# Kernel tuning notes

Hardware: AMD Instinct MI355X
Metric: run time of the kernel (lower is better)

The kernel has to match this reference:

```python
import jax, jax.numpy as jnp
import numpy as np

B, T, H, W, E, V, K = 16, 64, 16, 32, 256, 128, 3
NUM_BLOCKS = 3


def setup_inputs() -> dict:
    key = jax.random.key(0)
    ks = jax.random.split(key, 8)
    sc = 0.05  # keep logits moderate
    return {
        "encoder_output": jax.random.normal(ks[0], (B, H, W, E), jnp.float32),
        "decoder_input": jax.random.normal(ks[1], (B, H, W, E), jnp.float32),
        "labels": jax.random.randint(ks[2], (B, T), 0, V),
        "embed_table": (jax.random.normal(ks[3], (V, E), jnp.float32) * sc),
        "conv_w": (jax.random.normal(ks[4], (K, E, 2 * E), jnp.float32) * sc),  # ConvTBC weight [k, Cin, Cout]
        "conv_b": jnp.zeros((2 * E,), jnp.float32),
        "W_w": (jax.random.normal(ks[5], (E, E), jnp.float32) * sc),   # Linear(out/2 -> E), torch layout [out,in]
        "W_b": jnp.zeros((E,), jnp.float32),
        "Wo_w": (jax.random.normal(ks[6], (V, E), jnp.float32) * sc),  # Linear(E -> V)
        "Wo_b": jnp.zeros((V,), jnp.float32),
    }


def reference(encoder_output, decoder_input, embed_table, conv_w, conv_b,
              W_w, W_b, Wo_w, Wo_b, labels):
    # Work in [B, T, C]; the torch code's TBC transposes are layout-only.
    s = embed_table[labels]                     # [B, T, E]  (s in original, kept fixed)
    a = s                                       # a_l
    dec_flat = decoder_input.reshape(B, H * W, E)            # [B, HW, E]
    residual = (encoder_output + decoder_input).reshape(B, H * W, E)  # [B, HW, E]

    for _ in range(NUM_BLOCKS):
        # ConvTBC: 1D conv over T, weight [k, Cin, Cout]
        conv = jax.lax.conv_general_dilated(
            a, conv_w, window_strides=(1,), padding=((K // 2, K // 2),),
            dimension_numbers=("NWC", "WIO", "NWC")) + conv_b   # [B, T, 2E]
        # GLU over channel dim
        za, zb = jnp.split(conv, 2, axis=-1)
        z = za * jax.nn.sigmoid(zb)                              # [B, T, E]
        h = z @ W_w.T + W_b + s                                  # [B, T, E]
        # exp / sum over spatial positions == softmax over HW (same math, stable)
        scores = jnp.einsum("bte,bse->bts", h, dec_flat)         # [B, T, HW]
        alpha = jax.nn.softmax(scores, axis=2)
        # weighted sum of residual (avoids the [B,T,HW,E] repeat)
        c = jnp.einsum("bts,bse->bte", alpha, residual)          # [B, T, E]
        a = c + z

    logits = a @ Wo_w.T + Wo_b                                   # [B, T, V]
    return jax.nn.log_softmax(logits, axis=2)


if __name__ == "__main__":
    out = reference(**setup_inputs())
    print(out.shape)
```

## Files before the change

kernel.cpp:

```cpp
#include <hip/hip_runtime.h>
#include <hip/hip_bf16.h>
#include <math.h>

#define BB 16
#define TT 64
#define HWXY 512
#define EE 256
#define VV 128

typedef __bf16 bf16x8 __attribute__((ext_vector_type(8)));
typedef unsigned short u16x8 __attribute__((ext_vector_type(8)));
typedef float f32x4 __attribute__((ext_vector_type(4)));
typedef unsigned short u16;

__device__ __forceinline__ f32x4 mfma16(bf16x8 a, bf16x8 b, f32x4 c) {
    return __builtin_amdgcn_mfma_f32_16x16x32_bf16(a, b, c, 0, 0, 0);
}

__device__ __forceinline__ unsigned short f2bf(float f) {
    union { float f; unsigned int i; } v; v.f = f;
    unsigned int x = v.i;
    return (unsigned short)((x + 0x7fffu + ((x >> 16) & 1u)) >> 16);
}

__device__ __forceinline__ float bf2f(unsigned short u) {
    union { unsigned int i; float f; } v; v.i = ((unsigned int)u) << 16;
    return v.f;
}

__device__ __forceinline__ u16x8 pack8(float4 v0, float4 v1) {
    u16x8 o;
    o[0] = f2bf(v0.x); o[1] = f2bf(v0.y); o[2] = f2bf(v0.z); o[3] = f2bf(v0.w);
    o[4] = f2bf(v1.x); o[5] = f2bf(v1.y); o[6] = f2bf(v1.z); o[7] = f2bf(v1.w);
    return o;
}

__device__ __forceinline__ void dma16(const void* g, void* l) {
    __builtin_amdgcn_global_load_lds(
        (const __attribute__((address_space(1))) void*)g,
        (__attribute__((address_space(3))) void*)l, 16, 0, 0);
}

#define VMWAIT0() do { asm volatile("s_waitcnt vmcnt(0)" ::: "memory"); \
                       __builtin_amdgcn_sched_barrier(0); } while (0)

__global__ __launch_bounds__(256) void k_setup(
    const float* __restrict__ enc, const float* __restrict__ dec,
    const int* __restrict__ labels, const float* __restrict__ embed,
    const float* __restrict__ conv_w, const float* __restrict__ W_w,
    const float* __restrict__ Wo_w,
    u16* __restrict__ s_bf, u16* __restrict__ dec_bf, u16* __restrict__ resT,
    u16* __restrict__ convwT, u16* __restrict__ WT, u16* __restrict__ Wo_bf) {
    __shared__ unsigned short tl[64][66];
    int bid = blockIdx.x;
    if (bid < 512) {
        const int b = bid >> 5, rem = bid & 31;
        const int s0 = (rem >> 2) << 6, e0 = (rem & 3) << 6;
#pragma unroll
        for (int it = 0; it < 16; ++it) {
            int lin = threadIdx.x + it * 256;
            int sl = lin >> 6, el = lin & 63;
            int src = (b * HWXY + s0 + sl) * EE + e0 + el;
            float dv = dec[src];
            dec_bf[src] = f2bf(dv);
            tl[sl][el] = f2bf(enc[src] + dv);
        }
        __syncthreads();
#pragma unroll
        for (int it = 0; it < 16; ++it) {
            int lin = threadIdx.x + it * 256;
            int el = lin >> 6, sl = lin & 63;
            resT[(b * EE + e0 + el) * HWXY + s0 + sl] = tl[sl][el];
        }
        return;
    }
    bid -= 512;
    if (bid < 96) {
        const int c0 = (bid >> 3) << 6, j0 = (bid & 7) << 6;
#pragma unroll
        for (int it = 0; it < 16; ++it) {
            int lin = threadIdx.x + it * 256;
            int cl = lin >> 6, jl = lin & 63;
            tl[cl][jl] = f2bf(conv_w[(c0 + cl) * 512 + j0 + jl]);
        }
        __syncthreads();
#pragma unroll
        for (int it = 0; it < 16; ++it) {
            int lin = threadIdx.x + it * 256;
            int jl = lin >> 6, cl = lin & 63;
            convwT[(j0 + jl) * 768 + c0 + cl] = tl[cl][jl];
        }
        return;
    }
    bid -= 96;
    if (bid < 16) {
        const int c0 = (bid >> 2) << 6, j0 = (bid & 3) << 6;
#pragma unroll
        for (int it = 0; it < 16; ++it) {
            int lin = threadIdx.x + it * 256;
            int cl = lin >> 6, jl = lin & 63;
            tl[cl][jl] = f2bf(W_w[(c0 + cl) * 256 + j0 + jl]);
        }
        __syncthreads();
#pragma unroll
        for (int it = 0; it < 16; ++it) {
            int lin = threadIdx.x + it * 256;
            int el = lin >> 6, pl = lin & 63;
            WT[(j0 + el) * 256 + c0 + pl] = tl[pl][el];
        }
        return;
    }
    bid -= 16;
    int i8 = (bid * 256 + threadIdx.x) * 8;
    const int n1 = BB * TT * EE;
    if (i8 < n1) {
        int b = i8 >> 14, t = (i8 >> 8) & 63, e = i8 & 255;
        int lab = labels[b * TT + t];
        const float* ep = embed + lab * EE + e;
        float4 v0 = *(const float4*)ep, v1 = *(const float4*)(ep + 4);
        *(u16x8*)(s_bf + i8) = pack8(v0, v1);
        return;
    }
    i8 -= n1;
    float4 v0 = *(const float4*)(Wo_w + i8), v1 = *(const float4*)(Wo_w + i8 + 4);
    *(u16x8*)(Wo_bf + i8) = pack8(v0, v1);
}

__global__ __launch_bounds__(256) void k_precomp(
    const u16* __restrict__ dec_bf, const u16* __restrict__ WT,
    const u16* __restrict__ s_bf, const float* __restrict__ W_b,
    u16* __restrict__ G, float* __restrict__ base_g,
    const u16* __restrict__ convwT, const float* __restrict__ conv_b,
    u16* __restrict__ z_bf) {
    __shared__ __align__(16) char smem[98304];
    char* const As = smem;
    char* const Bs = smem + 32768;
    const int tid = threadIdx.x;
    const int w = tid >> 6, L = tid & 63, l16 = L & 15, lg = L >> 4;
    int bid = blockIdx.x;

    if (bid < 256) {
        const int b = bid >> 4, st = (bid >> 1) & 7, et = bid & 1;
#pragma unroll
        for (int i = 0; i < 8; ++i) {
            const int p = w * 8 + i;
            const int r = 2 * p + (L >> 5);
            dma16(dec_bf + (b * HWXY + st * 64 + r) * EE + (((L & 31) ^ (r & 7)) << 3),
                  As + p * 1024);
        }
#pragma unroll
        for (int i = 0; i < 16; ++i) {
            const int slot = w * 16 + i;
            const int kc = slot >> 3, nf = slot & 7;
            dma16(WT + (et * 128 + nf * 16 + l16) * EE + kc * 32 + lg * 8,
                  Bs + slot * 1024);
        }
        VMWAIT0();
        __syncthreads();
        f32x4 acc[4][2] = {{{0,0,0,0},{0,0,0,0}},{{0,0,0,0},{0,0,0,0}},
                           {{0,0,0,0},{0,0,0,0}},{{0,0,0,0},{0,0,0,0}}};
#pragma unroll
        for (int kc = 0; kc < 8; ++kc) {
#pragma unroll
            for (int m = 0; m < 4; ++m) {
                const int arow = m * 16 + l16;
                const bf16x8 af = *(const bf16x8*)(
                    As + arow * 512 + (((kc * 4 + lg) ^ (arow & 7)) << 4));
                acc[m][0] = mfma16(af, *(const bf16x8*)(Bs + (kc * 8 + w * 2) * 1024 + L * 16), acc[m][0]);
                acc[m][1] = mfma16(af, *(const bf16x8*)(Bs + (kc * 8 + w * 2 + 1) * 1024 + L * 16), acc[m][1]);
            }
        }
#pragma unroll
        for (int m = 0; m < 4; ++m)
#pragma unroll
            for (int nf = 0; nf < 2; ++nf)
#pragma unroll
                for (int j = 0; j < 4; ++j) {
                    const int s = st * 64 + m * 16 + lg * 4 + j;
                    const int e = et * 128 + w * 32 + nf * 16 + l16;
                    G[(b * HWXY + s) * EE + e] = f2bf(acc[m][nf][j]);
                }
        return;
    }
    if (bid < 384) {
        bid -= 256;
        const int b = bid >> 3, st = bid & 7;
#pragma unroll
        for (int it = 0; it < 8; ++it) {
            int unit = tid + it * 256;
            int row = unit >> 5, ch = unit & 31;
            u16x8 v = *(const u16x8*)(s_bf + (b * TT + row) * EE + ch * 8);
            u16x8 o;
#pragma unroll
            for (int k = 0; k < 8; ++k) o[k] = f2bf(bf2f(v[k]) + W_b[ch * 8 + k]);
            *(u16x8*)(As + row * 512 + ((ch ^ (row & 7)) << 4)) = o;
        }
#pragma unroll
        for (int i = 0; i < 8; ++i) {
            const int slot = w * 8 + i;
            const int kc = slot >> 2, nf = slot & 3;
            dma16(dec_bf + (b * HWXY + st * 64 + nf * 16 + l16) * EE + kc * 32 + lg * 8,
                  Bs + slot * 1024);
        }
        VMWAIT0();
        __syncthreads();
        f32x4 acc[4] = {{0,0,0,0},{0,0,0,0},{0,0,0,0},{0,0,0,0}};
        const int arow = w * 16 + l16;
#pragma unroll
        for (int kc = 0; kc < 8; ++kc) {
            const bf16x8 af = *(const bf16x8*)(
                As + arow * 512 + (((kc * 4 + lg) ^ (arow & 7)) << 4));
#pragma unroll
            for (int nf = 0; nf < 4; ++nf)
                acc[nf] = mfma16(af, *(const bf16x8*)(Bs + (kc * 4 + nf) * 1024 + L * 16), acc[nf]);
        }
#pragma unroll
        for (int nf = 0; nf < 4; ++nf)
#pragma unroll
            for (int j = 0; j < 4; ++j) {
                const int t = w * 16 + lg * 4 + j;
                base_g[(b * TT + t) * HWXY + st * 64 + nf * 16 + l16] = acc[nf][j];
            }
        return;
    }
    {
        bid -= 384;
        const int ct = bid >> 4, b = bid & 15;
        char* const Ac = smem;
        char* const Bc = smem + 33792;
#pragma unroll
        for (int i = 0; i < 12; ++i) {
            const int slot = w * 12 + i;
            const int kc = slot >> 1, half = slot & 1;
            dma16(convwT + (ct * 16 + l16 + half * 256) * 768 + kc * 32 + lg * 8,
                  Bc + slot * 1024);
        }
#pragma unroll
        for (int i = 0; i < 8; ++i) {
            const int p = w * 8 + i;
            const int r = 1 + 2 * p + (L >> 5);
            dma16(s_bf + (b * TT + r - 1) * EE + (((L & 31) ^ (r & 7)) << 3),
                  Ac + 512 + p * 1024);
        }
        if (tid < 64) {
            char* dst = (tid < 32) ? (Ac + tid * 16) : (Ac + 65 * 512 + (tid - 32) * 16);
            *(u16x8*)dst = (u16x8){0,0,0,0,0,0,0,0};
        }
        VMWAIT0();
        __syncthreads();

        f32x4 za = {0,0,0,0}, zb = {0,0,0,0};
#pragma unroll
        for (int kt = 0; kt < 3; ++kt) {
            const int arow = w * 16 + l16 + kt;
            const char* ab = Ac + arow * 512;
            const int swz = (arow & 7) << 4;
#pragma unroll
            for (int ec = 0; ec < 8; ++ec) {
                const bf16x8 af = *(const bf16x8*)(ab + ((ec * 64 + lg * 16) ^ swz));
                const int kc = kt * 8 + ec;
                za = mfma16(af, *(const bf16x8*)(Bc + (kc * 2) * 1024 + L * 16), za);
                zb = mfma16(af, *(const bf16x8*)(Bc + (kc * 2 + 1) * 1024 + L * 16), zb);
            }
        }
        const int p = ct * 16 + l16;
        const float cbA = conv_b[p], cbB = conv_b[p + 256];
#pragma unroll
        for (int j = 0; j < 4; ++j) {
            const int t = w * 16 + lg * 4 + j;
            const float v = za[j] + cbA, u = zb[j] + cbB;
            z_bf[(b * TT + t) * EE + p] = f2bf(v / (1.0f + __expf(-u)));
        }
    }
}

__global__ __launch_bounds__(256) void k_conv(
    const u16* __restrict__ a_in, const u16* __restrict__ convwT,
    const float* __restrict__ conv_b, u16* __restrict__ z_bf) {
    __shared__ __align__(16) char As[33792];
    __shared__ __align__(16) char Bs[49152];
    const int b = blockIdx.x, ct = blockIdx.y;
    const int tid = threadIdx.x;
    const int w = tid >> 6, L = tid & 63, l16 = L & 15, lg = L >> 4;

#pragma unroll
    for (int i = 0; i < 12; ++i) {
        const int slot = w * 12 + i;
        const int kc = slot >> 1, half = slot & 1;
        dma16(convwT + (ct * 16 + l16 + half * 256) * 768 + kc * 32 + lg * 8,
              Bs + slot * 1024);
    }
#pragma unroll
    for (int i = 0; i < 8; ++i) {
        const int p = w * 8 + i;
        const int r = 1 + 2 * p + (L >> 5);
        dma16(a_in + (b * TT + r - 1) * EE + (((L & 31) ^ (r & 7)) << 3),
              As + 512 + p * 1024);
    }
    if (tid < 64) {
        char* dst = (tid < 32) ? (As + tid * 16) : (As + 65 * 512 + (tid - 32) * 16);
        *(u16x8*)dst = (u16x8){0,0,0,0,0,0,0,0};
    }
    VMWAIT0();
    __syncthreads();

    f32x4 za = {0,0,0,0}, zb = {0,0,0,0};
#pragma unroll
    for (int kt = 0; kt < 3; ++kt) {
        const int arow = w * 16 + l16 + kt;
        const char* ab = As + arow * 512;
        const int swz = (arow & 7) << 4;
#pragma unroll
        for (int ec = 0; ec < 8; ++ec) {
            const bf16x8 af = *(const bf16x8*)(ab + ((ec * 64 + lg * 16) ^ swz));
            const int kc = kt * 8 + ec;
            za = mfma16(af, *(const bf16x8*)(Bs + (kc * 2) * 1024 + L * 16), za);
            zb = mfma16(af, *(const bf16x8*)(Bs + (kc * 2 + 1) * 1024 + L * 16), zb);
        }
    }
    const int p = ct * 16 + l16;
    const float cbA = conv_b[p], cbB = conv_b[p + 256];
#pragma unroll
    for (int j = 0; j < 4; ++j) {
        const int t = w * 16 + lg * 4 + j;
        const float v = za[j] + cbA, u = zb[j] + cbB;
        z_bf[(b * TT + t) * EE + p] = f2bf(v / (1.0f + __expf(-u)));
    }
}

__global__ __launch_bounds__(256) void k_scores(
    const u16* __restrict__ z_bf, const u16* __restrict__ G,
    const float* __restrict__ base_g, u16* __restrict__ p_bf,
    float* __restrict__ m_part, float* __restrict__ s_part) {
    __shared__ __align__(16) char Zs[32768];
    __shared__ __align__(16) char Gs[16384];
    __shared__ float basel[64 * 36];
    const int b = blockIdx.x, st = blockIdx.y;
    const int tid = threadIdx.x;
    const int w = tid >> 6, L = tid & 63, l16 = L & 15, lg = L >> 4;

#pragma unroll
    for (int i = 0; i < 8; ++i) {
        const int p = w * 8 + i;
        const int r = 2 * p + (L >> 5);
        dma16(z_bf + (b * TT + r) * EE + (((L & 31) ^ (r & 7)) << 3), Zs + p * 1024);
    }
#pragma unroll
    for (int i = 0; i < 4; ++i) {
        const int slot = w * 4 + i;
        const int kc = slot >> 1, nf = slot & 1;
        dma16(G + (b * HWXY + st * 32 + nf * 16 + l16) * EE + kc * 32 + lg * 8,
              Gs + slot * 1024);
    }
    {
        const int row = tid >> 2, c0 = (tid & 3) * 8;
        const float* src = base_g + (b * TT + row) * HWXY + st * 32 + c0;
        float4 v0 = *(const float4*)src, v1 = *(const float4*)(src + 4);
        *(float4*)(basel + row * 36 + c0) = v0;
        *(float4*)(basel + row * 36 + c0 + 4) = v1;
    }
    VMWAIT0();
    __syncthreads();

    f32x4 sc[2] = {{0,0,0,0},{0,0,0,0}};
    const int arow = w * 16 + l16;
#pragma unroll
    for (int kc = 0; kc < 8; ++kc) {
        const bf16x8 af = *(const bf16x8*)(
            Zs + arow * 512 + (((kc * 4 + lg) ^ (arow & 7)) << 4));
        sc[0] = mfma16(af, *(const bf16x8*)(Gs + (kc * 2) * 1024 + L * 16), sc[0]);
        sc[1] = mfma16(af, *(const bf16x8*)(Gs + (kc * 2 + 1) * 1024 + L * 16), sc[1]);
    }
    float pm[4], ps[4];
#pragma unroll
    for (int j = 0; j < 4; ++j) {
        const int row = w * 16 + lg * 4 + j;
        sc[0][j] += basel[row * 36 + l16];
        sc[1][j] += basel[row * 36 + 16 + l16];
        float m = fmaxf(sc[0][j], sc[1][j]);
#pragma unroll
        for (int off = 8; off >= 1; off >>= 1) m = fmaxf(m, __shfl_xor(m, off));
        pm[j] = m;
        const float p0 = __expf(sc[0][j] - m);
        const float p1 = __expf(sc[1][j] - m);
        sc[0][j] = p0; sc[1][j] = p1;
        float s = p0 + p1;
#pragma unroll
        for (int off = 8; off >= 1; off >>= 1) s += __shfl_xor(s, off);
        ps[j] = s;
    }
    if (l16 == 0) {
#pragma unroll
        for (int j = 0; j < 4; ++j) {
            const int t = w * 16 + lg * 4 + j;
            m_part[(b * 16 + st) * TT + t] = pm[j];
            s_part[(b * 16 + st) * TT + t] = ps[j];
        }
    }
#pragma unroll
    for (int nf = 0; nf < 2; ++nf)
#pragma unroll
        for (int j = 0; j < 4; ++j) {
            const int t = w * 16 + lg * 4 + j;
            p_bf[(b * TT + t) * HWXY + st * 32 + nf * 16 + l16] = f2bf(sc[nf][j]);
        }
}

__global__ __launch_bounds__(256) void k_attn(
    const u16* __restrict__ p_bf, const u16* __restrict__ resT,
    const u16* __restrict__ z_bf, const float* __restrict__ m_part,
    const float* __restrict__ s_part, u16* __restrict__ a_out) {
    __shared__ __align__(16) char Ps[32768];
    __shared__ __align__(16) char Bs[32768];
    __shared__ u16 Zr[1024];
    __shared__ float mp[512], sp[512];
    const int b = blockIdx.x, et = blockIdx.y, tt = blockIdx.z;
    const int tid = threadIdx.x;
    const int w = tid >> 6, L = tid & 63, l16 = L & 15, lg = L >> 4;

#pragma unroll
    for (int i = 0; i < 8; ++i) {
        const int r = w * 8 + i;
        dma16(p_bf + (b * TT + tt * 32 + r) * HWXY + ((L ^ (r & 7)) << 3), Ps + r * 1024);
    }
#pragma unroll
    for (int i = 0; i < 8; ++i) {
        const int slot = w * 8 + i;
        const int kc = slot >> 1, nf = slot & 1;
        dma16(resT + (b * EE + et * 32 + nf * 16 + l16) * HWXY + kc * 32 + lg * 8,
              Bs + slot * 1024);
    }
    {
        if (tid < 128) {
            const int t = tid >> 2, part = tid & 3;
            *(u16x8*)(Zr + t * 32 + part * 8) =
                *(const u16x8*)(z_bf + (b * TT + tt * 32 + t) * EE + et * 32 + part * 8);
        }
        const int stl = tid >> 5, tl = tid & 31;
        mp[tid] = m_part[(b * 16 + stl) * TT + tt * 32 + tl];
        sp[tid] = s_part[(b * 16 + stl) * TT + tt * 32 + tl];
        mp[tid + 256] = m_part[(b * 16 + stl + 8) * TT + tt * 32 + tl];
        sp[tid + 256] = s_part[(b * 16 + stl + 8) * TT + tt * 32 + tl];
    }
    VMWAIT0();
    __syncthreads();

    const int mg = w >> 1, nh = w & 1;
    float corr[4][16];
#pragma unroll
    for (int j = 0; j < 4; ++j) {
        const int row = mg * 16 + lg * 4 + j;
        float mgl = mp[row];
#pragma unroll
        for (int s = 1; s < 16; ++s) mgl = fmaxf(mgl, mp[s * 32 + row]);
        float S = 0.f;
#pragma unroll
        for (int s = 0; s < 16; ++s) {
            const float c = __expf(mp[s * 32 + row] - mgl);
            corr[j][s] = c;
            S += sp[s * 32 + row] * c;
        }
        const float is = 1.0f / S;
#pragma unroll
        for (int s = 0; s < 16; ++s) corr[j][s] *= is;
    }

    f32x4 ca = {0,0,0,0};
    const int arow = mg * 16 + l16;
#pragma unroll
    for (int st = 0; st < 16; ++st) {
        const bf16x8 af = *(const bf16x8*)(
            Ps + arow * 1024 + (((st * 4 + lg) ^ (arow & 7)) << 4));
        f32x4 t0 = mfma16(af, *(const bf16x8*)(Bs + (st * 2 + nh) * 1024 + L * 16),
                          (f32x4){0,0,0,0});
#pragma unroll
        for (int j = 0; j < 4; ++j) ca[j] += t0[j] * corr[j][st];
    }
#pragma unroll
    for (int j = 0; j < 4; ++j) {
        const int row = mg * 16 + lg * 4 + j;
        const int t = tt * 32 + row;
        a_out[(b * TT + t) * EE + et * 32 + nh * 16 + l16] =
            f2bf(ca[j] + bf2f(Zr[row * 32 + nh * 16 + l16]));
    }
}

__global__ __launch_bounds__(256) void k_logits(
    const u16* __restrict__ a_bf, const u16* __restrict__ Wo_bf,
    const float* __restrict__ Wo_b, float* __restrict__ out) {
    __shared__ __align__(16) char As[8192];
    __shared__ __align__(16) char Ws[65536];
    __shared__ float red_m[64], red_s[64];
    const int b = blockIdx.x, tt = blockIdx.y;
    const int tid = threadIdx.x;
    const int w = tid >> 6, L = tid & 63, l16 = L & 15, lg = L >> 4;

#pragma unroll
    for (int i = 0; i < 2; ++i) {
        const int p = w * 2 + i;
        const int row = p * 2 + (L >> 5);
        dma16(a_bf + (b * TT + tt * 16 + row) * EE + (((L & 31) ^ (row & 7)) << 3),
              As + p * 1024);
    }
#pragma unroll
    for (int i = 0; i < 16; ++i) {
        const int slot = w * 16 + i;
        const int kc = slot >> 3, vg = slot & 7;
        dma16(Wo_bf + (vg * 16 + l16) * EE + kc * 32 + lg * 8, Ws + slot * 1024);
    }
    VMWAIT0();
    __syncthreads();

    f32x4 l0 = {0,0,0,0}, l1 = {0,0,0,0};
#pragma unroll
    for (int kc = 0; kc < 8; ++kc) {
        const bf16x8 af = *(const bf16x8*)(As + l16 * 512 + ((kc * 64 + lg * 16) ^ ((l16 & 7) << 4)));
        l0 = mfma16(af, *(const bf16x8*)(Ws + (kc * 8 + w * 2) * 1024 + L * 16), l0);
        l1 = mfma16(af, *(const bf16x8*)(Ws + (kc * 8 + w * 2 + 1) * 1024 + L * 16), l1);
    }
    const int v0 = w * 32 + l16, v1 = v0 + 16;
    const float wb0 = Wo_b[v0], wb1 = Wo_b[v1];
    float lv0[4], lv1[4], mg[4];
#pragma unroll
    for (int j = 0; j < 4; ++j) {
        lv0[j] = l0[j] + wb0;
        lv1[j] = l1[j] + wb1;
        float m = fmaxf(lv0[j], lv1[j]);
#pragma unroll
        for (int off = 8; off >= 1; off >>= 1) m = fmaxf(m, __shfl_xor(m, off));
        if (l16 == 0) red_m[(lg * 4 + j) * 4 + w] = m;
    }
    __syncthreads();
#pragma unroll
    for (int j = 0; j < 4; ++j) {
        const int row = lg * 4 + j;
        float m = red_m[row * 4 + 0];
#pragma unroll
        for (int ww = 1; ww < 4; ++ww) m = fmaxf(m, red_m[row * 4 + ww]);
        mg[j] = m;
        float s = __expf(lv0[j] - m) + __expf(lv1[j] - m);
#pragma unroll
        for (int off = 8; off >= 1; off >>= 1) s += __shfl_xor(s, off);
        if (l16 == 0) red_s[row * 4 + w] = s;
    }
    __syncthreads();
#pragma unroll
    for (int j = 0; j < 4; ++j) {
        const int row = lg * 4 + j;
        float s = red_s[row * 4 + 0] + red_s[row * 4 + 1] + red_s[row * 4 + 2] + red_s[row * 4 + 3];
        const float lse = mg[j] + __logf(s);
        const int gt = b * TT + tt * 16 + row;
        out[gt * VV + v0] = lv0[j] - lse;
        out[gt * VV + v1] = lv1[j] - lse;
    }
}

extern "C" void kernel_launch(void* const* d_in, const int* in_sizes, int n_in,
                              void* d_out, int out_size, void* d_ws, size_t ws_size,
                              hipStream_t stream) {
    const float* enc    = (const float*)d_in[0];
    const float* dec    = (const float*)d_in[1];
    const int*   labels = (const int*)d_in[2];
    const float* embed  = (const float*)d_in[3];
    const float* conv_w = (const float*)d_in[4];
    const float* conv_b = (const float*)d_in[5];
    const float* W_w    = (const float*)d_in[6];
    const float* W_b    = (const float*)d_in[7];
    const float* Wo_w   = (const float*)d_in[8];
    const float* Wo_b   = (const float*)d_in[9];
    float* out = (float*)d_out;
    char* ws = (char*)d_ws;

    u16*   a0     = (u16*)(ws + 0x000000);
    u16*   a1     = (u16*)(ws + 0x080000);
    u16*   s_bf   = (u16*)(ws + 0x100000);
    u16*   dec_bf = (u16*)(ws + 0x180000);
    u16*   resT   = (u16*)(ws + 0x580000);
    u16*   convwT = (u16*)(ws + 0x980000);
    u16*   WT     = (u16*)(ws + 0xA40000);
    u16*   Wo_bf  = (u16*)(ws + 0xA60000);
    u16*   z_bf   = (u16*)(ws + 0xA80000);
    u16*   p_bf   = (u16*)(ws + 0xB00000);
    float* m_part = (float*)(ws + 0xC00000);
    float* s_part = (float*)(ws + 0xC10000);
    float* base_g = (float*)(ws + 0xC20000);
    u16*   G      = (u16*)(ws + 0xE20000);

    k_setup<<<768, 256, 0, stream>>>(enc, dec, labels, embed, conv_w, W_w, Wo_w,
                                     s_bf, dec_bf, resT, convwT, WT, Wo_bf);
    k_precomp<<<640, 256, 0, stream>>>(dec_bf, WT, s_bf, W_b, G, base_g,
                                       convwT, conv_b, z_bf);

    k_scores<<<dim3(16, 16), 256, 0, stream>>>(z_bf, G, base_g, p_bf, m_part, s_part);
    k_attn<<<dim3(16, 8, 2), 256, 0, stream>>>(p_bf, resT, z_bf, m_part, s_part, a1);

    k_conv<<<dim3(16, 16), 256, 0, stream>>>(a1, convwT, conv_b, z_bf);
    k_scores<<<dim3(16, 16), 256, 0, stream>>>(z_bf, G, base_g, p_bf, m_part, s_part);
    k_attn<<<dim3(16, 8, 2), 256, 0, stream>>>(p_bf, resT, z_bf, m_part, s_part, a0);

    k_conv<<<dim3(16, 16), 256, 0, stream>>>(a0, convwT, conv_b, z_bf);
    k_scores<<<dim3(16, 16), 256, 0, stream>>>(z_bf, G, base_g, p_bf, m_part, s_part);
    k_attn<<<dim3(16, 8, 2), 256, 0, stream>>>(p_bf, resT, z_bf, m_part, s_part, a1);

    k_logits<<<dim3(16, 4), 256, 0, stream>>>(a1, Wo_bf, Wo_b, out);
}
```

Before: 66.31 us.

## Fuse scores, softmax and attention into one flash-style kernel per block

Replaces the separate scores and attention kernels with one kernel. Each workgroup handles 16 time steps of one batch over all 512 spatial positions. It computes the scores, does the full softmax in registers with cross-wave reductions through LDS, then multiplies by the residual, double-buffering G and resT tiles with async global-to-LDS loads. This removes the p_bf, m_part and s_part round trips through global memory and three kernel launches. The cost is a grid of only 64 workgroups with about 107KB of LDS each, so most of the GPU's compute units sit idle.

Result: slower. 95.41 us (+43.9%).

```diff
diff --git a/kernel.cpp b/kernel.cpp
--- a/kernel.cpp
+++ b/kernel.cpp
@@ -41,8 +41,13 @@
         (__attribute__((address_space(3))) void*)l, 16, 0, 0);
 }
 
-#define VMWAIT0() do { asm volatile("s_waitcnt vmcnt(0)" ::: "memory"); \
+#define VMWAIT(N) do { asm volatile("s_waitcnt vmcnt(" #N ")" ::: "memory"); \
                        __builtin_amdgcn_sched_barrier(0); } while (0)
+#define VMWAIT0() VMWAIT(0)
+
+__device__ __forceinline__ void frag_store(char* lds, int col, int row, unsigned short v) {
+    *(unsigned short*)(lds + ((col >> 3) << 8) + row * 16 + ((col & 7) << 1)) = v;
+}
 
 __global__ __launch_bounds__(256) void k_setup(
     const float* __restrict__ enc, const float* __restrict__ dec,
@@ -328,160 +333,144 @@
     }
 }
 
-__global__ __launch_bounds__(256) void k_scores(
+__global__ __launch_bounds__(256) void k_sattn(
     const u16* __restrict__ z_bf, const u16* __restrict__ G,
-    const float* __restrict__ base_g, u16* __restrict__ p_bf,
-    float* __restrict__ m_part, float* __restrict__ s_part) {
-    __shared__ __align__(16) char Zs[32768];
-    __shared__ __align__(16) char Gs[16384];
-    __shared__ float basel[64 * 36];
-    const int b = blockIdx.x, st = blockIdx.y;
+    const float* __restrict__ base_g, const u16* __restrict__ resT,
+    u16* __restrict__ a_out) {
+    __shared__ __align__(16) char smem[107008];
+    char* const zs = smem;
+    float* const red_m = (float*)(smem + 8192);
+    float* const red_s = (float*)(smem + 8448);
+    char* const pb = smem + 8704;
+    char* const big = smem + 41472;
+
+    const int b = blockIdx.x, t0 = blockIdx.y << 4;
     const int tid = threadIdx.x;
     const int w = tid >> 6, L = tid & 63, l16 = L & 15, lg = L >> 4;
-
-#pragma unroll
-    for (int i = 0; i < 8; ++i) {
-        const int p = w * 8 + i;
-        const int r = 2 * p + (L >> 5);
-        dma16(z_bf + (b * TT + r) * EE + (((L & 31) ^ (r & 7)) << 3), Zs + p * 1024);
-    }
-#pragma unroll
-    for (int i = 0; i < 4; ++i) {
-        const int slot = w * 4 + i;
-        const int kc = slot >> 1, nf = slot & 1;
-        dma16(G + (b * HWXY + st * 32 + nf * 16 + l16) * EE + kc * 32 + lg * 8,
-              Gs + slot * 1024);
-    }
-    {
-        const int row = tid >> 2, c0 = (tid & 3) * 8;
-        const float* src = base_g + (b * TT + row) * HWXY + st * 32 + c0;
-        float4 v0 = *(const float4*)src, v1 = *(const float4*)(src + 4);
-        *(float4*)(basel + row * 36 + c0) = v0;
-        *(float4*)(basel + row * 36 + c0 + 4) = v1;
-    }
-    VMWAIT0();
-    __syncthreads();
-
-    f32x4 sc[2] = {{0,0,0,0},{0,0,0,0}};
-    const int arow = w * 16 + l16;
-#pragma unroll
-    for (int kc = 0; kc < 8; ++kc) {
-        const bf16x8 af = *(const bf16x8*)(
-            Zs + arow * 512 + (((kc * 4 + lg) ^ (arow & 7)) << 4));
-        sc[0] = mfma16(af, *(const bf16x8*)(Gs + (kc * 2) * 1024 + L * 16), sc[0]);
-        sc[1] = mfma16(af, *(const bf16x8*)(Gs + (kc * 2 + 1) * 1024 + L * 16), sc[1]);
-    }
-    float pm[4], ps[4];
-#pragma unroll
-    for (int j = 0; j < 4; ++j) {
-        const int row = w * 16 + lg * 4 + j;
-        sc[0][j] += basel[row * 36 + l16];
-        sc[1][j] += basel[row * 36 + 16 + l16];
-        float m = fmaxf(sc[0][j], sc[1][j]);
+    char* const myg = big + w * 8192;
+
+    dma16(z_bf + (b * TT + t0 + l16) * EE + (w * 2) * 32 + lg * 8, zs + (w * 2) * 1024);
+    dma16(z_bf + (b * TT + t0 + l16) * EE + (w * 2 + 1) * 32 + lg * 8, zs + (w * 2 + 1) * 1024);
+#pragma unroll
+    for (int c = 0; c < 8; ++c)
+        dma16(base_g + (b * TT + t0 + (L >> 2)) * HWXY + c * 64 + w * 16 + (L & 3) * 4,
+              pb + c * 4096 + w * 1024);
+#pragma unroll
+    for (int c = 0; c < 2; ++c)
+#pragma unroll
+        for (int kc = 0; kc < 8; ++kc)
+            dma16(G + (b * HWXY + c * 64 + w * 16 + l16) * EE + kc * 32 + lg * 8,
+                  myg + c * 32768 + kc * 1024);
+    VMWAIT(16);
+    __syncthreads();
+
+    f32x4 sc[8] = {{0,0,0,0},{0,0,0,0},{0,0,0,0},{0,0,0,0},
+                   {0,0,0,0},{0,0,0,0},{0,0,0,0},{0,0,0,0}};
+#pragma unroll
+    for (int c = 0; c < 8; ++c) {
+        if (c < 7) { VMWAIT(8); } else { VMWAIT(0); }
+#pragma unroll
+        for (int kc = 0; kc < 8; ++kc) {
+            const bf16x8 af = *(const bf16x8*)(zs + kc * 1024 + L * 16);
+            const bf16x8 bfr = *(const bf16x8*)(myg + (c & 1) * 32768 + kc * 1024 + L * 16);
+            sc[c] = mfma16(af, bfr, sc[c]);
+        }
+        if (c < 6)
+#pragma unroll
+            for (int kc = 0; kc < 8; ++kc)
+                dma16(G + (b * HWXY + (c + 2) * 64 + w * 16 + l16) * EE + kc * 32 + lg * 8,
+                      myg + (c & 1) * 32768 + kc * 1024);
+    }
+#pragma unroll
+    for (int c = 0; c < 8; ++c)
+#pragma unroll
+        for (int j = 0; j < 4; ++j)
+            sc[c][j] += *(const float*)(pb + c * 4096 + w * 1024 +
+                                        (lg * 4 + j) * 64 + (l16 >> 2) * 16 + (l16 & 3) * 4);
+#pragma unroll
+    for (int c = 0; c < 2; ++c)
+#pragma unroll
+        for (int q = 0; q < 8; ++q) {
+            const int kc = q >> 2, nf = q & 3;
+            dma16(resT + (b * EE + w * 64 + nf * 16 + l16) * HWXY + c * 64 + kc * 32 + lg * 8,
+                  myg + c * 32768 + q * 1024);
+        }
+
+#pragma unroll
+    for (int j = 0; j < 4; ++j) {
+        float m = sc[0][j];
+#pragma unroll
+        for (int c = 1; c < 8; ++c) m = fmaxf(m, sc[c][j]);
 #pragma unroll
         for (int off = 8; off >= 1; off >>= 1) m = fmaxf(m, __shfl_xor(m, off));
-        pm[j] = m;
-        const float p0 = __expf(sc[0][j] - m);
-        const float p1 = __expf(sc[1][j] - m);
-        sc[0][j] = p0; sc[1][j] = p1;
-        float s = p0 + p1;
+        if (l16 == 0) red_m[(lg * 4 + j) * 4 + w] = m;
+    }
+    __syncthreads();
+    float inv[4];
+#pragma unroll
+    for (int j = 0; j < 4; ++j) {
+        const int row = lg * 4 + j;
+        const float m = fmaxf(fmaxf(red_m[row * 4 + 0], red_m[row * 4 + 1]),
+                              fmaxf(red_m[row * 4 + 2], red_m[row * 4 + 3]));
+        float s = 0.f;
+#pragma unroll
+        for (int c = 0; c < 8; ++c) {
+            const float p = __expf(sc[c][j] - m);
+            sc[c][j] = p;
+            s += p;
+        }
 #pragma unroll
         for (int off = 8; off >= 1; off >>= 1) s += __shfl_xor(s, off);
-        ps[j] = s;
-    }
-    if (l16 == 0) {
+        if (l16 == 0) red_s[row * 4 + w] = s;
+    }
+    __syncthreads();
+#pragma unroll
+    for (int j = 0; j < 4; ++j) {
+        const int row = lg * 4 + j;
+        inv[j] = 1.0f / (red_s[row * 4 + 0] + red_s[row * 4 + 1] +
+                         red_s[row * 4 + 2] + red_s[row * 4 + 3]);
+    }
+#pragma unroll
+    for (int c = 0; c < 8; ++c) {
+        const int col = c * 64 + w * 16 + l16;
+#pragma unroll
+        for (int j = 0; j < 4; ++j)
+            frag_store(pb, col, lg * 4 + j, f2bf(sc[c][j]));
+    }
+    __syncthreads();
+
+    f32x4 acc[4] = {{0,0,0,0},{0,0,0,0},{0,0,0,0},{0,0,0,0}};
+#pragma unroll
+    for (int c = 0; c < 8; ++c) {
+        if (c < 7) { VMWAIT(8); } else { VMWAIT(0); }
+#pragma unroll
+        for (int kc = 0; kc < 2; ++kc) {
+            const bf16x8 af = *(const bf16x8*)(pb + (c * 2 + kc) * 1024 + L * 16);
+#pragma unroll
+            for (int nf = 0; nf < 4; ++nf) {
+                const bf16x8 bfr = *(const bf16x8*)(
+                    myg + (c & 1) * 32768 + (kc * 4 + nf) * 1024 + L * 16);
+                acc[nf] = mfma16(af, bfr, acc[nf]);
+            }
+        }
+        if (c < 6)
+#pragma unroll
+            for (int q = 0; q < 8; ++q) {
+                const int kc = q >> 2, nf = q & 3;
+                dma16(resT + (b * EE + w * 64 + nf * 16 + l16) * HWXY + (c + 2) * 64 + kc * 32 + lg * 8,
+                      myg + (c & 1) * 32768 + q * 1024);
+            }
+    }
+
+#pragma unroll
+    for (int nf = 0; nf < 4; ++nf) {
+        const int e = w * 64 + nf * 16 + l16;
 #pragma unroll
         for (int j = 0; j < 4; ++j) {
-            const int t = w * 16 + lg * 4 + j;
-            m_part[(b * 16 + st) * TT + t] = pm[j];
-            s_part[(b * 16 + st) * TT + t] = ps[j];
-        }
-    }
-#pragma unroll
-    for (int nf = 0; nf < 2; ++nf)
-#pragma unroll
-        for (int j = 0; j < 4; ++j) {
-            const int t = w * 16 + lg * 4 + j;
-            p_bf[(b * TT + t) * HWXY + st * 32 + nf * 16 + l16] = f2bf(sc[nf][j]);
-        }
-}
-
-__global__ __launch_bounds__(256) void k_attn(
-    const u16* __restrict__ p_bf, const u16* __restrict__ resT,
-    const u16* __restrict__ z_bf, const float* __restrict__ m_part,
-    const float* __restrict__ s_part, u16* __restrict__ a_out) {
-    __shared__ __align__(16) char Ps[32768];
-    __shared__ __align__(16) char Bs[32768];
-    __shared__ u16 Zr[1024];
-    __shared__ float mp[512], sp[512];
-    const int b = blockIdx.x, et = blockIdx.y, tt = blockIdx.z;
-    const int tid = threadIdx.x;
-    const int w = tid >> 6, L = tid & 63, l16 = L & 15, lg = L >> 4;
-
-#pragma unroll
-    for (int i = 0; i < 8; ++i) {
-        const int r = w * 8 + i;
-        dma16(p_bf + (b * TT + tt * 32 + r) * HWXY + ((L ^ (r & 7)) << 3), Ps + r * 1024);
-    }
-#pragma unroll
-    for (int i = 0; i < 8; ++i) {
-        const int slot = w * 8 + i;
-        const int kc = slot >> 1, nf = slot & 1;
-        dma16(resT + (b * EE + et * 32 + nf * 16 + l16) * HWXY + kc * 32 + lg * 8,
-              Bs + slot * 1024);
-    }
-    {
-        if (tid < 128) {
-            const int t = tid >> 2, part = tid & 3;
-            *(u16x8*)(Zr + t * 32 + part * 8) =
-                *(const u16x8*)(z_bf + (b * TT + tt * 32 + t) * EE + et * 32 + part * 8);
-        }
-        const int stl = tid >> 5, tl = tid & 31;
-        mp[tid] = m_part[(b * 16 + stl) * TT + tt * 32 + tl];
-        sp[tid] = s_part[(b * 16 + stl) * TT + tt * 32 + tl];
-        mp[tid + 256] = m_part[(b * 16 + stl + 8) * TT + tt * 32 + tl];
-        sp[tid + 256] = s_part[(b * 16 + stl + 8) * TT + tt * 32 + tl];
-    }
-    VMWAIT0();
-    __syncthreads();
-
-    const int mg = w >> 1, nh = w & 1;
-    float corr[4][16];
-#pragma unroll
-    for (int j = 0; j < 4; ++j) {
-        const int row = mg * 16 + lg * 4 + j;
-        float mgl = mp[row];
-#pragma unroll
-        for (int s = 1; s < 16; ++s) mgl = fmaxf(mgl, mp[s * 32 + row]);
-        float S = 0.f;
-#pragma unroll
-        for (int s = 0; s < 16; ++s) {
-            const float c = __expf(mp[s * 32 + row] - mgl);
-            corr[j][s] = c;
-            S += sp[s * 32 + row] * c;
-        }
-        const float is = 1.0f / S;
-#pragma unroll
-        for (int s = 0; s < 16; ++s) corr[j][s] *= is;
-    }
-
-    f32x4 ca = {0,0,0,0};
-    const int arow = mg * 16 + l16;
-#pragma unroll
-    for (int st = 0; st < 16; ++st) {
-        const bf16x8 af = *(const bf16x8*)(
-            Ps + arow * 1024 + (((st * 4 + lg) ^ (arow & 7)) << 4));
-        f32x4 t0 = mfma16(af, *(const bf16x8*)(Bs + (st * 2 + nh) * 1024 + L * 16),
-                          (f32x4){0,0,0,0});
-#pragma unroll
-        for (int j = 0; j < 4; ++j) ca[j] += t0[j] * corr[j][st];
-    }
-#pragma unroll
-    for (int j = 0; j < 4; ++j) {
-        const int row = mg * 16 + lg * 4 + j;
-        const int t = tt * 32 + row;
-        a_out[(b * TT + t) * EE + et * 32 + nh * 16 + l16] =
-            f2bf(ca[j] + bf2f(Zr[row * 32 + nh * 16 + l16]));
+            const int row = lg * 4 + j;
+            const float zv = bf2f(*(const u16*)(zs + ((e >> 3) << 8) + row * 16 + ((e & 7) << 1)));
+            a_out[(b * TT + t0 + row) * EE + e] = f2bf(acc[nf][j] * inv[j] + zv);
+        }
     }
 }
 
@@ -580,9 +569,6 @@
     u16*   WT     = (u16*)(ws + 0xA40000);
     u16*   Wo_bf  = (u16*)(ws + 0xA60000);
     u16*   z_bf   = (u16*)(ws + 0xA80000);
-    u16*   p_bf   = (u16*)(ws + 0xB00000);
-    float* m_part = (float*)(ws + 0xC00000);
-    float* s_part = (float*)(ws + 0xC10000);
     float* base_g = (float*)(ws + 0xC20000);
     u16*   G      = (u16*)(ws + 0xE20000);
 
@@ -591,16 +577,11 @@
     k_precomp<<<640, 256, 0, stream>>>(dec_bf, WT, s_bf, W_b, G, base_g,
                                        convwT, conv_b, z_bf);
 
-    k_scores<<<dim3(16, 16), 256, 0, stream>>>(z_bf, G, base_g, p_bf, m_part, s_part);
-    k_attn<<<dim3(16, 8, 2), 256, 0, stream>>>(p_bf, resT, z_bf, m_part, s_part, a1);
-
+    k_sattn<<<dim3(16, 4), 256, 0, stream>>>(z_bf, G, base_g, resT, a1);
     k_conv<<<dim3(16, 16), 256, 0, stream>>>(a1, convwT, conv_b, z_bf);
-    k_scores<<<dim3(16, 16), 256, 0, stream>>>(z_bf, G, base_g, p_bf, m_part, s_part);
-    k_attn<<<dim3(16, 8, 2), 256, 0, stream>>>(p_bf, resT, z_bf, m_part, s_part, a0);
-
+    k_sattn<<<dim3(16, 4), 256, 0, stream>>>(z_bf, G, base_g, resT, a0);
     k_conv<<<dim3(16, 16), 256, 0, stream>>>(a0, convwT, conv_b, z_bf);
-    k_scores<<<dim3(16, 16), 256, 0, stream>>>(z_bf, G, base_g, p_bf, m_part, s_part);
-    k_attn<<<dim3(16, 8, 2), 256, 0, stream>>>(p_bf, resT, z_bf, m_part, s_part, a1);
+    k_sattn<<<dim3(16, 4), 256, 0, stream>>>(z_bf, G, base_g, resT, a1);
 
     k_logits<<<dim3(16, 4), 256, 0, stream>>>(a1, Wo_bf, Wo_b, out);
 }
```
